# Performance work log

Hardware: AMD Instinct MI355X
Metric: run time of the kernel (lower is better)

The kernel has to match this reference:

```python
import jax, jax.numpy as jnp
import numpy as np
from jax import lax

GLIMPSE = 64
SCALES = (2, 4)


def _extract_patch(image, location, size):
    """image: [B,C,H,W] (H==W), location: [B,2] xy in [-1,1] -> [B,C,size,size]."""
    B, C, H, W = image.shape
    image_size = W
    pad = size // 2
    padded = jnp.pad(image, ((0, 0), (0, 0), (pad, pad), (pad, pad)))  # constant 0
    # start index per sample (x, y); .long() in torch -> truncation toward 0,
    # values here are non-negative so floor == trunc.
    start = (0.5 * ((location + 1.0) * (image_size - 1))).astype(jnp.int32)  # [B,2]

    def crop(img, st):
        # torch: padded[b, :, start_y:start_y+size, start_x:start_x+size]
        return lax.dynamic_slice(img, (0, st[1], st[0]), (C, size, size))

    return jax.vmap(crop)(padded, start)


def _glimpse(img0, img2, img4, location):
    scale_imgs = {0: img0, 2: img2, 4: img4}
    B, C = img0.shape[0], img0.shape[1]
    windows = [_extract_patch(scale_imgs[0], location, GLIMPSE)]
    for scale in SCALES:
        patch = _extract_patch(scale_imgs[scale], location, int(GLIMPSE * scale))
        # torchvision VF.resize: bilinear, half-pixel (align_corners=False), antialias
        patch = jax.image.resize(patch, (B, C, GLIMPSE, GLIMPSE), method='bilinear', antialias=True)
        if patch.shape[1] == 1:  # grayscale-only max-normalization
            mx = jnp.max(patch.reshape(B, -1), axis=-1)[:, None, None, None]
            patch = patch / (mx + 1e-6)
        windows.append(patch)
    return jnp.stack(windows, axis=1)  # [B, S, C, G, G]


def setup_inputs() -> dict:
    key = jax.random.key(0)
    k0, k2, k4, kl = jax.random.split(key, 4)
    B, C, HW = 64, 3, 512
    return {
        'img0': jax.random.uniform(k0, (B, C, HW, HW), dtype=jnp.float32),
        'img2': jax.random.uniform(k2, (B, C, HW, HW), dtype=jnp.float32),
        'img4': jax.random.uniform(k4, (B, C, HW, HW), dtype=jnp.float32),
        'location': jax.random.uniform(kl, (B, 2), minval=-1.0, maxval=1.0, dtype=jnp.float32),
    }


def reference(img0, img2, img4, location):
    return _glimpse(img0, img2, img4, location)
```

## Files before the change

kernel.cpp:

```cpp
#include <hip/hip_runtime.h>

#define HW 512
#define G 64

__device__ __forceinline__ void taps_s2(int o, int* idx, float* w) {
    if (o == 0) {
        idx[0] = 0; idx[1] = 0; idx[2] = 1; idx[3] = 2;
        w[0] = 0.0f; w[1] = 3.0f / 7.0f; w[2] = 3.0f / 7.0f; w[3] = 1.0f / 7.0f;
    } else if (o == 63) {
        idx[0] = 125; idx[1] = 126; idx[2] = 127; idx[3] = 127;
        w[0] = 1.0f / 7.0f; w[1] = 3.0f / 7.0f; w[2] = 3.0f / 7.0f; w[3] = 0.0f;
    } else {
        int base = 2 * o - 1;
        idx[0] = base; idx[1] = base + 1; idx[2] = base + 2; idx[3] = base + 3;
        w[0] = 0.125f; w[1] = 0.375f; w[2] = 0.375f; w[3] = 0.125f;
    }
}

__device__ __forceinline__ void taps_s4(int o, int* idx, float* w) {
    if (o == 0) {
        const float inv = 1.0f / 28.0f;
        const float ww[8] = {0.f, 0.f, 5.f, 7.f, 7.f, 5.f, 3.f, 1.f};
        const int  ii[8] = {0, 0, 0, 1, 2, 3, 4, 5};
        #pragma unroll
        for (int i = 0; i < 8; i++) { idx[i] = ii[i]; w[i] = ww[i] * inv; }
    } else if (o == 63) {
        const float inv = 1.0f / 28.0f;
        const float ww[8] = {1.f, 3.f, 5.f, 7.f, 7.f, 5.f, 0.f, 0.f};
        const int  ii[8] = {250, 251, 252, 253, 254, 255, 255, 255};
        #pragma unroll
        for (int i = 0; i < 8; i++) { idx[i] = ii[i]; w[i] = ww[i] * inv; }
    } else {
        const float inv = 1.0f / 32.0f;
        const float ww[8] = {1.f, 3.f, 5.f, 7.f, 7.f, 5.f, 3.f, 1.f};
        int base = 4 * o - 2;
        #pragma unroll
        for (int i = 0; i < 8; i++) { idx[i] = base + i; w[i] = ww[i] * inv; }
    }
}

__global__ __launch_bounds__(256) void glimpse_kernel(
    const float* __restrict__ img0,
    const float* __restrict__ img2,
    const float* __restrict__ img4,
    const float* __restrict__ loc,
    float* __restrict__ out)
{
    __shared__ float v[8192];

    const int t = threadIdx.x;
    const int blk = blockIdx.x;
    int s, bc, half = 0;
    if (blk < 384)      { s = 2; bc = blk >> 1; half = blk & 1; }
    else if (blk < 576) { s = 1; bc = blk - 384; }
    else                { s = 0; bc = blk - 576; }
    const int b = bc / 3;

    const float lx = loc[2 * b];
    const float ly = loc[2 * b + 1];
    const int stx = (int)(0.5f * ((lx + 1.0f) * 511.0f));
    const int sty = (int)(0.5f * ((ly + 1.0f) * 511.0f));

    float* outp = out + (((size_t)(b * 3 + s) * 3 + (bc - b * 3)) * G) * G;

    if (s == 0) {
        const float* img = img0 + (size_t)bc * HW * HW;
        #pragma unroll
        for (int i = 0; i < 16; i++) {
            int n = i * 256 + t;
            int oy = n >> 6, ox = n & 63;
            int gy = sty + oy - 32, gx = stx + ox - 32;
            float val = 0.0f;
            if (gy >= 0 && gy < HW && gx >= 0 && gx < HW)
                val = img[gy * HW + gx];
            outp[n] = val;
        }
        return;
    }

    if (s == 1) {
        const float* img = img2 + (size_t)bc * HW * HW;
        const int col = t & 127;
        const int gx = stx - 64 + col;
        const bool xok = (gx >= 0 && gx < HW);
        #pragma unroll 4
        for (int i = 0; i < 32; i++) {
            int n = i * 256 + t;
            int oy = n >> 7;
            float acc = 0.0f;
            if (xok) {
                int ri[4]; float rw[4];
                taps_s2(oy, ri, rw);
                #pragma unroll
                for (int k = 0; k < 4; k++) {
                    int gy = sty - 64 + ri[k];
                    if (gy >= 0 && gy < HW) acc += rw[k] * img[gy * HW + gx];
                }
            }
            v[n] = acc;
        }
        __syncthreads();
        #pragma unroll 4
        for (int i = 0; i < 16; i++) {
            int m = i * 256 + t;
            int ox = m & 63, oy = m >> 6;
            int xi[4]; float xw[4];
            taps_s2(ox, xi, xw);
            float acc = 0.0f;
            #pragma unroll
            for (int k = 0; k < 4; k++) acc += xw[k] * v[oy * 128 + xi[k]];
            outp[m] = acc;
        }
        return;
    }

    const float* img = img4 + (size_t)bc * HW * HW;
    const int oy0 = half * 32;
    {
        const int col = t;
        const int gx = stx - 128 + col;
        const bool xok = (gx >= 0 && gx < HW);
        #pragma unroll 4
        for (int i = 0; i < 32; i++) {
            int oy = oy0 + i;
            float acc = 0.0f;
            if (xok) {
                int ri[8]; float rw[8];
                taps_s4(oy, ri, rw);
                #pragma unroll
                for (int k = 0; k < 8; k++) {
                    int gy = sty - 128 + ri[k];
                    if (gy >= 0 && gy < HW) acc += rw[k] * img[gy * HW + gx];
                }
            }
            v[i * 256 + col] = acc;
        }
    }
    __syncthreads();
    #pragma unroll 4
    for (int i = 0; i < 8; i++) {
        int m = i * 256 + t;
        int ox = m & 63, oyl = m >> 6;
        int xi[8]; float xw[8];
        taps_s4(ox, xi, xw);
        float acc = 0.0f;
        #pragma unroll
        for (int k = 0; k < 8; k++) acc += xw[k] * v[oyl * 256 + xi[k]];
        outp[(size_t)(oy0 + oyl) * G + ox] = acc;
    }
}

extern "C" void kernel_launch(void* const* d_in, const int* in_sizes, int n_in,
                              void* d_out, int out_size, void* d_ws, size_t ws_size,
                              hipStream_t stream) {
    const float* img0 = (const float*)d_in[0];
    const float* img2 = (const float*)d_in[1];
    const float* img4 = (const float*)d_in[2];
    const float* loc  = (const float*)d_in[3];
    float* out = (float*)d_out;

    glimpse_kernel<<<dim3(768), dim3(256), 0, stream>>>(img0, img2, img4, loc, out);
}
```

Before: 487.4 us.

## Split glimpse work across more blocks and make tap loads branchless

Raises the block count by splitting the scale-2 path into 2 row slices and the scale-4 path into 4, which halves shared memory per block and spreads work over more CUs. Replaces the table-based tap helpers with closed-form weights and clamped indices so every load is unconditional and out-of-range taps get zero weight. This aims to cut divergence and expose more memory parallelism. In exchange it issues redundant clamped loads and adds arithmetic per tap.

```diff
diff --git a/kernel.cpp b/kernel.cpp
--- a/kernel.cpp
+++ b/kernel.cpp
@@ -3,40 +3,8 @@
 #define HW 512
 #define G 64
 
-__device__ __forceinline__ void taps_s2(int o, int* idx, float* w) {
-    if (o == 0) {
-        idx[0] = 0; idx[1] = 0; idx[2] = 1; idx[3] = 2;
-        w[0] = 0.0f; w[1] = 3.0f / 7.0f; w[2] = 3.0f / 7.0f; w[3] = 1.0f / 7.0f;
-    } else if (o == 63) {
-        idx[0] = 125; idx[1] = 126; idx[2] = 127; idx[3] = 127;
-        w[0] = 1.0f / 7.0f; w[1] = 3.0f / 7.0f; w[2] = 3.0f / 7.0f; w[3] = 0.0f;
-    } else {
-        int base = 2 * o - 1;
-        idx[0] = base; idx[1] = base + 1; idx[2] = base + 2; idx[3] = base + 3;
-        w[0] = 0.125f; w[1] = 0.375f; w[2] = 0.375f; w[3] = 0.125f;
-    }
-}
-
-__device__ __forceinline__ void taps_s4(int o, int* idx, float* w) {
-    if (o == 0) {
-        const float inv = 1.0f / 28.0f;
-        const float ww[8] = {0.f, 0.f, 5.f, 7.f, 7.f, 5.f, 3.f, 1.f};
-        const int  ii[8] = {0, 0, 0, 1, 2, 3, 4, 5};
-        #pragma unroll
-        for (int i = 0; i < 8; i++) { idx[i] = ii[i]; w[i] = ww[i] * inv; }
-    } else if (o == 63) {
-        const float inv = 1.0f / 28.0f;
-        const float ww[8] = {1.f, 3.f, 5.f, 7.f, 7.f, 5.f, 0.f, 0.f};
-        const int  ii[8] = {250, 251, 252, 253, 254, 255, 255, 255};
-        #pragma unroll
-        for (int i = 0; i < 8; i++) { idx[i] = ii[i]; w[i] = ww[i] * inv; }
-    } else {
-        const float inv = 1.0f / 32.0f;
-        const float ww[8] = {1.f, 3.f, 5.f, 7.f, 7.f, 5.f, 3.f, 1.f};
-        int base = 4 * o - 2;
-        #pragma unroll
-        for (int i = 0; i < 8; i++) { idx[i] = base + i; w[i] = ww[i] * inv; }
-    }
+__device__ __forceinline__ int clampi(int x, int lo, int hi) {
+    return min(max(x, lo), hi);
 }
 
 __global__ __launch_bounds__(256) void glimpse_kernel(
@@ -46,107 +14,131 @@
     const float* __restrict__ loc,
     float* __restrict__ out)
 {
-    __shared__ float v[8192];
+    __shared__ float v[4096];
 
     const int t = threadIdx.x;
     const int blk = blockIdx.x;
-    int s, bc, half = 0;
-    if (blk < 384)      { s = 2; bc = blk >> 1; half = blk & 1; }
-    else if (blk < 576) { s = 1; bc = blk - 384; }
-    else                { s = 0; bc = blk - 576; }
+    int s, bc, slice = 0;
+    if (blk < 768)       { s = 2; bc = blk >> 2; slice = blk & 3; }
+    else if (blk < 1152) { s = 1; bc = (blk - 768) >> 1; slice = (blk - 768) & 1; }
+    else                 { s = 0; bc = blk - 1152; }
     const int b = bc / 3;
+    const int c = bc - 3 * b;
 
     const float lx = loc[2 * b];
     const float ly = loc[2 * b + 1];
     const int stx = (int)(0.5f * ((lx + 1.0f) * 511.0f));
     const int sty = (int)(0.5f * ((ly + 1.0f) * 511.0f));
 
-    float* outp = out + (((size_t)(b * 3 + s) * 3 + (bc - b * 3)) * G) * G;
+    float* outp = out + ((size_t)(b * 3 + s) * 3 + c) * (G * G);
 
     if (s == 0) {
-        const float* img = img0 + (size_t)bc * HW * HW;
+        const float* img = img0 + (size_t)bc * (HW * HW);
         #pragma unroll
         for (int i = 0; i < 16; i++) {
             int n = i * 256 + t;
             int oy = n >> 6, ox = n & 63;
             int gy = sty + oy - 32, gx = stx + ox - 32;
-            float val = 0.0f;
-            if (gy >= 0 && gy < HW && gx >= 0 && gx < HW)
-                val = img[gy * HW + gx];
-            outp[n] = val;
+            int gyc = clampi(gy, 0, HW - 1);
+            int gxc = clampi(gx, 0, HW - 1);
+            float val = img[gyc * HW + gxc];
+            outp[n] = (gy == gyc && gx == gxc) ? val : 0.0f;
         }
         return;
     }
 
     if (s == 1) {
-        const float* img = img2 + (size_t)bc * HW * HW;
+        const float* img = img2 + (size_t)bc * (HW * HW);
+        const int oy0 = slice * 32;
         const int col = t & 127;
-        const int gx = stx - 64 + col;
-        const bool xok = (gx >= 0 && gx < HW);
-        #pragma unroll 4
-        for (int i = 0; i < 32; i++) {
-            int n = i * 256 + t;
-            int oy = n >> 7;
+        const int th  = t >> 7;
+        const int gx  = stx - 64 + col;
+        const int gxc = clampi(gx, 0, HW - 1);
+        const float xv = (gx == gxc) ? 1.0f : 0.0f;
+        #pragma unroll 8
+        for (int i = 0; i < 16; i++) {
+            int r  = 2 * i + th;
+            int oy = oy0 + r;
+            float inv = (oy == 0 || oy == 63) ? (1.0f / 7.0f) : 0.125f;
+            int base = 2 * oy - 1;
             float acc = 0.0f;
-            if (xok) {
-                int ri[4]; float rw[4];
-                taps_s2(oy, ri, rw);
-                #pragma unroll
-                for (int k = 0; k < 4; k++) {
-                    int gy = sty - 64 + ri[k];
-                    if (gy >= 0 && gy < HW) acc += rw[k] * img[gy * HW + gx];
-                }
+            #pragma unroll
+            for (int k = 0; k < 4; k++) {
+                const float wt = (k == 0 || k == 3) ? 1.0f : 3.0f;
+                int ii  = base + k;
+                int iic = clampi(ii, 0, 127);
+                int gy  = sty - 64 + iic;
+                int gyc = clampi(gy, 0, HW - 1);
+                float w = (ii == iic && gy == gyc) ? wt * inv : 0.0f;
+                acc += w * img[gyc * HW + gxc];
             }
-            v[n] = acc;
+            v[r * 128 + col] = acc * xv;
         }
         __syncthreads();
-        #pragma unroll 4
-        for (int i = 0; i < 16; i++) {
-            int m = i * 256 + t;
-            int ox = m & 63, oy = m >> 6;
-            int xi[4]; float xw[4];
-            taps_s2(ox, xi, xw);
+        #pragma unroll
+        for (int i = 0; i < 8; i++) {
+            int m  = i * 256 + t;
+            int ox = m & 63;
+            int r  = m >> 6;
+            float inv = (ox == 0 || ox == 63) ? (1.0f / 7.0f) : 0.125f;
+            int base = 2 * ox - 1;
             float acc = 0.0f;
             #pragma unroll
-            for (int k = 0; k < 4; k++) acc += xw[k] * v[oy * 128 + xi[k]];
-            outp[m] = acc;
+            for (int k = 0; k < 4; k++) {
+                const float wt = (k == 0 || k == 3) ? 1.0f : 3.0f;
+                int ii  = base + k;
+                int iic = clampi(ii, 0, 127);
+                float w = (ii == iic) ? wt * inv : 0.0f;
+                acc += w * v[r * 128 + iic];
+            }
+            outp[(size_t)(oy0 + r) * G + ox] = acc;
         }
         return;
     }
 
-    const float* img = img4 + (size_t)bc * HW * HW;
-    const int oy0 = half * 32;
     {
+        const float* img = img4 + (size_t)bc * (HW * HW);
+        const int oy0 = slice * 16;
         const int col = t;
-        const int gx = stx - 128 + col;
-        const bool xok = (gx >= 0 && gx < HW);
-        #pragma unroll 4
-        for (int i = 0; i < 32; i++) {
+        const int gx  = stx - 128 + col;
+        const int gxc = clampi(gx, 0, HW - 1);
+        const float xv = (gx == gxc) ? 1.0f : 0.0f;
+        const float WT[8] = {1.f, 3.f, 5.f, 7.f, 7.f, 5.f, 3.f, 1.f};
+        #pragma unroll 8
+        for (int i = 0; i < 16; i++) {
             int oy = oy0 + i;
+            float inv = (oy == 0 || oy == 63) ? (1.0f / 28.0f) : (1.0f / 32.0f);
+            int base = 4 * oy - 2;
             float acc = 0.0f;
-            if (xok) {
-                int ri[8]; float rw[8];
-                taps_s4(oy, ri, rw);
-                #pragma unroll
-                for (int k = 0; k < 8; k++) {
-                    int gy = sty - 128 + ri[k];
-                    if (gy >= 0 && gy < HW) acc += rw[k] * img[gy * HW + gx];
-                }
+            #pragma unroll
+            for (int k = 0; k < 8; k++) {
+                int ii  = base + k;
+                int iic = clampi(ii, 0, 255);
+                int gy  = sty - 128 + iic;
+                int gyc = clampi(gy, 0, HW - 1);
+                float w = (ii == iic && gy == gyc) ? WT[k] * inv : 0.0f;
+                acc += w * img[gyc * HW + gxc];
             }
-            v[i * 256 + col] = acc;
+            v[i * 256 + col] = acc * xv;
         }
-    }
-    __syncthreads();
-    #pragma unroll 4
-    for (int i = 0; i < 8; i++) {
-        int m = i * 256 + t;
-        int ox = m & 63, oyl = m >> 6;
-        int xi[8]; float xw[8];
-        taps_s4(ox, xi, xw);
-        float acc = 0.0f;
+        __syncthreads();
         #pragma unroll
-        for (int k = 0; k < 8; k++) acc += xw[k] * v[oyl * 256 + xi[k]];
-        outp[(size_t)(oy0 + oyl) * G + ox] = acc;
+        for (int i = 0; i < 4; i++) {
+            int m  = i * 256 + t;
+            int ox = m & 63;
+            int r  = m >> 6;
+            float inv = (ox == 0 || ox == 63) ? (1.0f / 28.0f) : (1.0f / 32.0f);
+            int base = 4 * ox - 2;
+            float acc = 0.0f;
+            #pragma unroll
+            for (int k = 0; k < 8; k++) {
+                int ii  = base + k;
+                int iic = clampi(ii, 0, 255);
+                float w = (ii == iic) ? WT[k] * inv : 0.0f;
+                acc += w * v[r * 256 + iic];
+            }
+            outp[(size_t)(oy0 + r) * G + ox] = acc;
+        }
     }
 }
 
@@ -159,5 +151,5 @@
     const float* loc  = (const float*)d_in[3];
     float* out = (float*)d_out;
 
-    glimpse_kernel<<<dim3(768), dim3(256), 0, stream>>>(img0, img2, img4, loc, out);
+    glimpse_kernel<<<dim3(1344), dim3(256), 0, stream>>>(img0, img2, img4, loc, out);
 }
```

New measurement: 400.3 us. 1.22x faster.
